# Kernel optimization log

Measured on AMD Instinct MI355X. Metric: run time of the kernel, lower is better.

The kernel has to match this reference:

```python
import jax, jax.numpy as jnp
import numpy as np

WINDOW = 11
C1 = 0.01 ** 2
C2 = 0.03 ** 2
PAD = WINDOW // 2


def _box_filter(img, kernel):
    # img: [B,1,H,W], kernel: [1,1,w,w]; SAME padding (odd window)
    return jax.lax.conv_general_dilated(
        img, kernel,
        window_strides=(1, 1),
        padding=[(PAD, PAD), (PAD, PAD)],
        dimension_numbers=('NCHW', 'OIHW', 'NCHW'))


def setup_inputs() -> dict:
    key = jax.random.key(0)
    kx, ky = jax.random.split(key)
    B, C, H, W = 64, 1, 512, 512
    x = jax.random.uniform(kx, (B, C, H, W), dtype=jnp.float32)
    y = jax.random.uniform(ky, (B, C, H, W), dtype=jnp.float32)
    kernel = jnp.ones((1, 1, WINDOW, WINDOW), dtype=jnp.float32) / (WINDOW ** 2)
    return {"x": x, "y": y, "kernel": kernel}


def reference(x, y, kernel):
    mu_x = _box_filter(x, kernel)
    mu_y = _box_filter(y, kernel)
    mu_x2 = mu_x * mu_x
    mu_y2 = mu_y * mu_y
    mu_xy = mu_x * mu_y
    sigma_x2 = _box_filter(x * x, kernel) - mu_x2
    sigma_y2 = _box_filter(y * y, kernel) - mu_y2
    sigma_xy = _box_filter(x * y, kernel) - mu_xy
    ssim_map = ((2.0 * mu_xy + C1) * (2.0 * sigma_xy + C2)) / (
        (mu_x2 + mu_y2 + C1) * (sigma_x2 + sigma_y2 + C2))
    return 1.0 - jnp.mean(ssim_map)
```

## Files before the change

kernel.cpp:

```cpp
#include <hip/hip_runtime.h>
#include <stdint.h>


#define IMG_H 512
#define IMG_W 512
#define N_IMG 64
#define RAD   5
#define SH    16
#define NBANDG 8
#define NBLOCKS (N_IMG * NBANDG)

#define C1_SSIM 1.0e-4f
#define C2_SSIM 9.0e-4f

#define SLOT_BYTES 4096

typedef __attribute__((address_space(3))) uint32_t lds_u32_t;
typedef const __attribute__((address_space(1))) uint32_t glb_u32_t;

__device__ __forceinline__ void dma16(void* lds, const void* g) {
    __builtin_amdgcn_global_load_lds((glb_u32_t*)g, (lds_u32_t*)lds, 16, 0, 0);
}

__global__ __launch_bounds__(256) void ssim_fused(const float* __restrict__ x,
                                                  const float* __restrict__ y,
                                                  float* __restrict__ part)
{
    __shared__ __align__(16) char ring[4][2][SLOT_BYTES];

    const int tx  = threadIdx.x & 63;
    const int ts  = threadIdx.x >> 6;
    const int img = blockIdx.x >> 3;
    const int bg  = blockIdx.x & (NBANDG - 1);
    const int r0  = bg * (4 * SH) + ts * SH;
    const int c0  = tx * 8;

    const float* __restrict__ xi = x + (size_t)img * (IMG_H * IMG_W);
    const float* __restrict__ yi = y + (size_t)img * (IMG_H * IMG_W);

    auto dma_row = [&](char* s, int ri) -> float {
        int rc = ri < 0 ? 0 : (ri > IMG_H - 1 ? IMG_H - 1 : ri);
        float sc = (ri >= 0 && ri < IMG_H) ? 1.0f : 0.0f;
        const char* xg = (const char*)(xi + (size_t)rc * IMG_W) + tx * 16;
        const char* yg = (const char*)(yi + (size_t)rc * IMG_W) + tx * 16;
        dma16(s,        xg);
        dma16(s + 1024, xg + 1024);
        dma16(s + 2048, yg);
        dma16(s + 3072, yg + 1024);
        return sc;
    };

    float Vx[8], Vy[8], Vxx[8], Vyy[8], Vxy[8];
#pragma unroll
    for (int j = 0; j < 8; ++j) { Vx[j] = 0.f; Vy[j] = 0.f; Vxx[j] = 0.f; Vyy[j] = 0.f; Vxy[j] = 0.f; }

    auto accum_lds = [&](const char* s, float f) {
        const float4* xr = (const float4*)(s + (size_t)tx * 32);
        const float4* yr = (const float4*)(s + 2048 + (size_t)tx * 32);
        float4 x0 = xr[0], x1 = xr[1];
        float4 y0 = yr[0], y1 = yr[1];
        float xs[8] = {x0.x, x0.y, x0.z, x0.w, x1.x, x1.y, x1.z, x1.w};
        float ys[8] = {y0.x, y0.y, y0.z, y0.w, y1.x, y1.y, y1.z, y1.w};
#pragma unroll
        for (int j = 0; j < 8; ++j) {
            float fx = f * xs[j];
            float fy = f * ys[j];
            Vx[j] += fx;
            Vy[j] += fy;
            Vxx[j] = fmaf(fx, xs[j], Vxx[j]);
            Vyy[j] = fmaf(fy, ys[j], Vyy[j]);
            Vxy[j] = fmaf(fx, ys[j], Vxy[j]);
        }
    };

    auto hsum = [&](const float (&V)[8], float (&S)[8]) {
        float w[18];
#pragma unroll
        for (int k = 0; k < 5; ++k) {
            float l = __shfl_up(V[3 + k], 1, 64);
            w[k] = (tx == 0) ? 0.f : l;
        }
#pragma unroll
        for (int j = 0; j < 8; ++j) w[5 + j] = V[j];
#pragma unroll
        for (int k = 0; k < 5; ++k) {
            float r = __shfl_down(V[k], 1, 64);
            w[13 + k] = (tx == 63) ? 0.f : r;
        }
        float s = 0.f;
#pragma unroll
        for (int t = 0; t < 11; ++t) s += w[t];
        S[0] = s;
#pragma unroll
        for (int j = 1; j < 8; ++j) { s += w[j + 10] - w[j - 1]; S[j] = s; }
    };

    char* cur = &ring[ts][0][0];
    char* nxt = &ring[ts][1][0];

    float scCur = dma_row(cur, r0 - 5);
#pragma unroll 1
    for (int i = 0; i < 2 * RAD; ++i) {
        accum_lds(cur, scCur);
        float scN = dma_row(nxt, r0 - 4 + i);
        char* t = cur; cur = nxt; nxt = t;
        scCur = scN;
    }

    const float inv121 = 1.0f / 121.0f;
    float loss = 0.0f;

#pragma unroll 1
    for (int ro = r0; ro < r0 + SH; ++ro) {
        accum_lds(cur, scCur);
        float scN = dma_row(nxt, ro + 6);

        int  rs      = ro - RAD;
        bool haveSub = (rs >= 0);
        float4 sx0, sx1, sy0, sy1;
        if (haveSub) {
            const float4* xr = (const float4*)(xi + (size_t)rs * IMG_W + c0);
            const float4* yr = (const float4*)(yi + (size_t)rs * IMG_W + c0);
            sx0 = xr[0]; sx1 = xr[1]; sy0 = yr[0]; sy1 = yr[1];
        }

        float Sx[8], Sy[8], Sxx[8], Syy[8], Sxy[8];
        hsum(Vx,  Sx);
        hsum(Vy,  Sy);
        hsum(Vxx, Sxx);
        hsum(Vyy, Syy);
        hsum(Vxy, Sxy);

#pragma unroll
        for (int j = 0; j < 8; ++j) {
            float mx  = Sx[j] * inv121;
            float my  = Sy[j] * inv121;
            float mx2 = mx * mx;
            float my2 = my * my;
            float mxy = mx * my;
            float vx  = Sxx[j] * inv121 - mx2;
            float vy  = Syy[j] * inv121 - my2;
            float vxy = Sxy[j] * inv121 - mxy;
            float num = (2.0f * mxy + C1_SSIM) * (2.0f * vxy + C2_SSIM);
            float den = (mx2 + my2 + C1_SSIM) * (vx + vy + C2_SSIM);
            loss += __fdividef(num, den);
        }

        if (haveSub) {
            float xs[8] = {sx0.x, sx0.y, sx0.z, sx0.w, sx1.x, sx1.y, sx1.z, sx1.w};
            float ys[8] = {sy0.x, sy0.y, sy0.z, sy0.w, sy1.x, sy1.y, sy1.z, sy1.w};
#pragma unroll
            for (int j = 0; j < 8; ++j) {
                Vx[j]  -= xs[j];
                Vy[j]  -= ys[j];
                Vxx[j] = fmaf(-xs[j], xs[j], Vxx[j]);
                Vyy[j] = fmaf(-ys[j], ys[j], Vyy[j]);
                Vxy[j] = fmaf(-xs[j], ys[j], Vxy[j]);
            }
        }

        char* t = cur; cur = nxt; nxt = t;
        scCur = scN;
    }

#pragma unroll
    for (int off = 32; off > 0; off >>= 1)
        loss += __shfl_down(loss, off, 64);

    __shared__ float pr[4];
    if (tx == 0) pr[ts] = loss;
    __syncthreads();
    if (threadIdx.x == 0)
        part[blockIdx.x] = (pr[0] + pr[1]) + (pr[2] + pr[3]);
}

__global__ __launch_bounds__(256) void ssim_reduce(const float* __restrict__ part,
                                                   float* __restrict__ out)
{
    const int t  = threadIdx.x;
    const int tx = t & 63;
    float s = part[t] + part[t + 256];
#pragma unroll
    for (int off = 32; off > 0; off >>= 1)
        s += __shfl_down(s, off, 64);
    __shared__ float ws[4];
    if (tx == 0) ws[t >> 6] = s;
    __syncthreads();
    if (t == 0) {
        float total = (ws[0] + ws[1]) + (ws[2] + ws[3]);
        out[0] = 1.0f - total * (1.0f / ((float)N_IMG * IMG_H * IMG_W));
    }
}

extern "C" void kernel_launch(void* const* d_in, const int* in_sizes, int n_in,
                              void* d_out, int out_size, void* d_ws, size_t ws_size,
                              hipStream_t stream) {
    const float* x = (const float*)d_in[0];
    const float* y = (const float*)d_in[1];
    float* part = (float*)d_ws;

    ssim_fused<<<NBLOCKS, 256, 0, stream>>>(x, y, part);
    ssim_reduce<<<1, 256, 0, stream>>>(part, (float*)d_out);
}
```

Measured before the change: 173.5 us.

## Double waves per block, merge x²+y² accumulators, swizzle block-to-band mapping

Each block now runs 8 waves of 8 output rows instead of 4 waves of 16, so there are twice as many waves in flight to hide memory latency. The price is more halo warm-up work per output row. The separate x² and y² running sums are merged into one accumulator, since SSIM only needs their sum. This removes one horizontal-sum pass and cuts register use. Block indices are also remapped so that neighbouring bands spread across XCDs, and the partial-sum scratch reuses the LDS ring buffer.

```diff
diff --git a/kernel.cpp b/kernel.cpp
--- a/kernel.cpp
+++ b/kernel.cpp
@@ -6,7 +6,8 @@
 #define IMG_W 512
 #define N_IMG 64
 #define RAD   5
-#define SH    16
+#define SH    8
+#define WAVES 8
 #define NBANDG 8
 #define NBLOCKS (N_IMG * NBANDG)
 
@@ -22,17 +23,19 @@
     __builtin_amdgcn_global_load_lds((glb_u32_t*)g, (lds_u32_t*)lds, 16, 0, 0);
 }
 
-__global__ __launch_bounds__(256) void ssim_fused(const float* __restrict__ x,
+__global__ __launch_bounds__(512) void ssim_fused(const float* __restrict__ x,
                                                   const float* __restrict__ y,
                                                   float* __restrict__ part)
 {
-    __shared__ __align__(16) char ring[4][2][SLOT_BYTES];
+    __shared__ __align__(16) char ring[WAVES][2][SLOT_BYTES];
 
     const int tx  = threadIdx.x & 63;
     const int ts  = threadIdx.x >> 6;
-    const int img = blockIdx.x >> 3;
-    const int bg  = blockIdx.x & (NBANDG - 1);
-    const int r0  = bg * (4 * SH) + ts * SH;
+
+    const int wid = (blockIdx.x & 7) * (NBLOCKS / 8) + (blockIdx.x >> 3);
+    const int img = wid >> 3;
+    const int bg  = wid & (NBANDG - 1);
+    const int r0  = bg * (WAVES * SH) + ts * SH;
     const int c0  = tx * 8;
 
     const float* __restrict__ xi = x + (size_t)img * (IMG_H * IMG_W);
@@ -50,9 +53,9 @@
         return sc;
     };
 
-    float Vx[8], Vy[8], Vxx[8], Vyy[8], Vxy[8];
-#pragma unroll
-    for (int j = 0; j < 8; ++j) { Vx[j] = 0.f; Vy[j] = 0.f; Vxx[j] = 0.f; Vyy[j] = 0.f; Vxy[j] = 0.f; }
+    float Vx[8], Vy[8], Vss[8], Vxy[8];
+#pragma unroll
+    for (int j = 0; j < 8; ++j) { Vx[j] = 0.f; Vy[j] = 0.f; Vss[j] = 0.f; Vxy[j] = 0.f; }
 
     auto accum_lds = [&](const char* s, float f) {
         const float4* xr = (const float4*)(s + (size_t)tx * 32);
@@ -67,8 +70,8 @@
             float fy = f * ys[j];
             Vx[j] += fx;
             Vy[j] += fy;
-            Vxx[j] = fmaf(fx, xs[j], Vxx[j]);
-            Vyy[j] = fmaf(fy, ys[j], Vyy[j]);
+            Vss[j] = fmaf(fx, xs[j], Vss[j]);
+            Vss[j] = fmaf(fy, ys[j], Vss[j]);
             Vxy[j] = fmaf(fx, ys[j], Vxy[j]);
         }
     };
@@ -124,11 +127,10 @@
             sx0 = xr[0]; sx1 = xr[1]; sy0 = yr[0]; sy1 = yr[1];
         }
 
-        float Sx[8], Sy[8], Sxx[8], Syy[8], Sxy[8];
+        float Sx[8], Sy[8], Sss[8], Sxy[8];
         hsum(Vx,  Sx);
         hsum(Vy,  Sy);
-        hsum(Vxx, Sxx);
-        hsum(Vyy, Syy);
+        hsum(Vss, Sss);
         hsum(Vxy, Sxy);
 
 #pragma unroll
@@ -138,11 +140,10 @@
             float mx2 = mx * mx;
             float my2 = my * my;
             float mxy = mx * my;
-            float vx  = Sxx[j] * inv121 - mx2;
-            float vy  = Syy[j] * inv121 - my2;
+            float vs  = Sss[j] * inv121 - mx2 - my2;
             float vxy = Sxy[j] * inv121 - mxy;
             float num = (2.0f * mxy + C1_SSIM) * (2.0f * vxy + C2_SSIM);
-            float den = (mx2 + my2 + C1_SSIM) * (vx + vy + C2_SSIM);
+            float den = (mx2 + my2 + C1_SSIM) * (vs + C2_SSIM);
             loss += __fdividef(num, den);
         }
 
@@ -153,8 +154,8 @@
             for (int j = 0; j < 8; ++j) {
                 Vx[j]  -= xs[j];
                 Vy[j]  -= ys[j];
-                Vxx[j] = fmaf(-xs[j], xs[j], Vxx[j]);
-                Vyy[j] = fmaf(-ys[j], ys[j], Vyy[j]);
+                Vss[j] = fmaf(-xs[j], xs[j], Vss[j]);
+                Vss[j] = fmaf(-ys[j], ys[j], Vss[j]);
                 Vxy[j] = fmaf(-xs[j], ys[j], Vxy[j]);
             }
         }
@@ -167,11 +168,15 @@
     for (int off = 32; off > 0; off >>= 1)
         loss += __shfl_down(loss, off, 64);
 
-    __shared__ float pr[4];
+    __syncthreads();
+    float* pr = reinterpret_cast<float*>(&ring[0][0][0]);
     if (tx == 0) pr[ts] = loss;
     __syncthreads();
-    if (threadIdx.x == 0)
-        part[blockIdx.x] = (pr[0] + pr[1]) + (pr[2] + pr[3]);
+    if (threadIdx.x == 0) {
+        float t = ((pr[0] + pr[1]) + (pr[2] + pr[3]))
+                + ((pr[4] + pr[5]) + (pr[6] + pr[7]));
+        part[blockIdx.x] = t;
+    }
 }
 
 __global__ __launch_bounds__(256) void ssim_reduce(const float* __restrict__ part,
@@ -199,6 +204,6 @@
     const float* y = (const float*)d_in[1];
     float* part = (float*)d_ws;
 
-    ssim_fused<<<NBLOCKS, 256, 0, stream>>>(x, y, part);
+    ssim_fused<<<NBLOCKS, 512, 0, stream>>>(x, y, part);
     ssim_reduce<<<1, 256, 0, stream>>>(part, (float*)d_out);
 }
```

After: 183.7 us. 1.06x slower.
